# Optimization experiments

Hardware: AMD Instinct MI355X
Metric: run time of the kernel (lower is better)

Reference implementation:

```python
import jax, jax.numpy as jnp
import numpy as np

EMB = 300
NUM_LAYERS = 5
NUM_GRAPHS = 1024
NUM_JUNCTIONS = 8192
TEMP = 0.04
EPS = 1e-5
SELF_LOOP_BOND_TYPE = 4


def gcn_conv(x, edge_index, edge_attr, W, b, ee1, ee2):
    # pretrain-gnns GCNConv: add self-loops (bond type 4, direction 0),
    # degree-normalized add aggregation of (x_src + edge_emb).
    N = x.shape[0]
    loop = jnp.arange(N, dtype=edge_index.dtype)
    src = jnp.concatenate([edge_index[0], loop])
    dst = jnp.concatenate([edge_index[1], loop])
    bt = jnp.concatenate([edge_attr[:, 0], jnp.full((N,), SELF_LOOP_BOND_TYPE, edge_attr.dtype)])
    bd = jnp.concatenate([edge_attr[:, 1], jnp.zeros((N,), edge_attr.dtype)])
    eemb = ee1[bt] + ee2[bd]                                   # [E+N, D]
    deg = jax.ops.segment_sum(jnp.ones(src.shape, x.dtype), src, num_segments=N)
    dinv = jnp.where(deg > 0, 1.0 / jnp.sqrt(jnp.maximum(deg, 1e-12)), 0.0)
    norm = dinv[src] * dinv[dst]                               # [E+N]
    h = x @ W.T + b                                            # [N, D]
    msg = norm[:, None] * (h[src] + eemb)                      # gather + fuse
    return jax.ops.segment_sum(msg, dst, num_segments=N)      # scatter-add


def batchnorm(h, gamma, beta):
    mu = h.mean(0)
    var = h.var(0)
    return gamma * (h - mu) / jnp.sqrt(var + EPS) + beta


def gnn_encoder(x, edge_index, edge_attr, ae1, ae2, W, b, ee1, ee2, gamma, beta):
    h = ae1[x[:, 0]] + ae2[x[:, 1]]
    for l in range(NUM_LAYERS):
        h = gcn_conv(h, edge_index, edge_attr, W[l], b[l], ee1[l], ee2[l])
        h = batchnorm(h, gamma[l], beta[l])
        if l < NUM_LAYERS - 1:
            h = jax.nn.relu(h)
    return h


def junction_encoder(h, jW, jb, jee1, jee2):
    # SuperEncoder is called with empty edge_index -> only self-loops.
    empty_ei = jnp.zeros((2, 0), jnp.int32)
    empty_ea = jnp.zeros((0, 2), jnp.int32)
    h = jax.nn.relu(gcn_conv(h, empty_ei, empty_ea, jW[0], jb[0], jee1[0], jee2[0]))
    return gcn_conv(h, empty_ei, empty_ea, jW[1], jb[1], jee1[1], jee2[1])


def mean_pool(h, ids, num):
    s = jax.ops.segment_sum(h, ids, num_segments=num)
    c = jax.ops.segment_sum(jnp.ones((h.shape[0],), h.dtype), ids, num_segments=num)
    return s / jnp.maximum(c, 1.0)[:, None]


def l2norm(h):
    return h / jnp.maximum(jnp.linalg.norm(h, axis=1, keepdims=True), 1e-12)


def setup_inputs() -> dict:
    key = jax.random.key(0)
    ks = jax.random.split(key, 32)
    N, E = 200000, 400000
    inp = {
        'batch_x': jax.random.randint(ks[0], (N, 2), 0, 3, jnp.int32),
        'batch_edge_index': jax.random.randint(ks[1], (2, E), 0, N, jnp.int32),
        'batch_edge_attr': jax.random.randint(ks[2], (E, 2), 0, 3, jnp.int32),
        'batch_graph_ids': jax.random.randint(ks[3], (N,), 0, NUM_GRAPHS, jnp.int32),
        'frag_x': jax.random.randint(ks[4], (N, 2), 0, 3, jnp.int32),
        'frag_edge_index': jax.random.randint(ks[5], (2, E), 0, N, jnp.int32),
        'frag_edge_attr': jax.random.randint(ks[6], (E, 2), 0, 3, jnp.int32),
        'frag_junction_ids': jax.random.randint(ks[7], (N,), 0, NUM_JUNCTIONS, jnp.int32),
        'junction_graph_ids': jax.random.randint(ks[8], (NUM_JUNCTIONS,), 0, NUM_GRAPHS, jnp.int32),
        'junction_mask': jax.random.uniform(ks[9], (NUM_JUNCTIONS,), jnp.float32),
    }
    s = 0.05
    inp.update({
        'atom_emb1': jax.random.normal(ks[10], (120, EMB), jnp.float32) * s,
        'atom_emb2': jax.random.normal(ks[11], (3, EMB), jnp.float32) * s,
        'gnn_W': jax.random.normal(ks[12], (NUM_LAYERS, EMB, EMB), jnp.float32) * s,
        'gnn_b': jnp.zeros((NUM_LAYERS, EMB), jnp.float32),
        'gnn_ee1': jax.random.normal(ks[13], (NUM_LAYERS, 6, EMB), jnp.float32) * s,
        'gnn_ee2': jax.random.normal(ks[14], (NUM_LAYERS, 3, EMB), jnp.float32) * s,
        'bn_gamma': jnp.ones((NUM_LAYERS, EMB), jnp.float32),
        'bn_beta': jnp.zeros((NUM_LAYERS, EMB), jnp.float32),
        'jct_W': jax.random.normal(ks[15], (2, EMB, EMB), jnp.float32) * s,
        'jct_b': jnp.zeros((2, EMB), jnp.float32),
        'jct_ee1': jax.random.normal(ks[16], (2, 6, EMB), jnp.float32) * s,
        'jct_ee2': jax.random.normal(ks[17], (2, 3, EMB), jnp.float32) * s,
        'mask_embedding': jax.random.normal(ks[18], (EMB,), jnp.float32),
    })
    return inp


def reference(batch_x, batch_edge_index, batch_edge_attr, batch_graph_ids,
              frag_x, frag_edge_index, frag_edge_attr, frag_junction_ids,
              junction_graph_ids, junction_mask,
              atom_emb1, atom_emb2, gnn_W, gnn_b, gnn_ee1, gnn_ee2,
              bn_gamma, bn_beta, jct_W, jct_b, jct_ee1, jct_ee2, mask_embedding):
    # branch 0: whole molecules
    h = gnn_encoder(batch_x, batch_edge_index, batch_edge_attr,
                    atom_emb1, atom_emb2, gnn_W, gnn_b, gnn_ee1, gnn_ee2, bn_gamma, bn_beta)
    g = mean_pool(h, batch_graph_ids, NUM_GRAPHS)
    f0 = l2norm(junction_encoder(g, jct_W, jct_b, jct_ee1, jct_ee2))
    # branch 1: fragments -> junction nodes, masked overwrite, pooled per graph
    h = gnn_encoder(frag_x, frag_edge_index, frag_edge_attr,
                    atom_emb1, atom_emb2, gnn_W, gnn_b, gnn_ee1, gnn_ee2, bn_gamma, bn_beta)
    j = mean_pool(h, frag_junction_ids, NUM_JUNCTIONS)
    j = jnp.where(junction_mask[:, None] > 0.5, mask_embedding[None, :], j)
    j = junction_encoder(j, jct_W, jct_b, jct_ee1, jct_ee2)
    f1 = l2norm(mean_pool(j, junction_graph_ids, NUM_GRAPHS))
    logits = (f0 @ f1.T) / TEMP
    return logits
```

## Files before the change

kernel.cpp:

```cpp
#include <hip/hip_runtime.h>
#include <math.h>

#define EMBD 300
#define HROW 304
#define LDF  304
#define KEXT 320
#define BCH  80
#define BSTR 40
#define TS2  312
#define CE(a,b) (((a)+(b)-1)/(b))

typedef _Float16 h16;
typedef __attribute__((ext_vector_type(8))) _Float16 half8;
typedef __attribute__((ext_vector_type(4))) float f32x4;

__global__ void k_diag(float* out, int n, float v){
  int i = blockIdx.x*256 + threadIdx.x;
  if (i < n) out[i] = v;
}
__global__ void k_set_val(int* p, int n, int v){
  int i = blockIdx.x*256 + threadIdx.x;
  if (i < n) p[i] = v;
}
__global__ void k_count_src(const int* __restrict__ ei, int E, int* __restrict__ deg){
  int e = blockIdx.x*256 + threadIdx.x;
  if (e < E) atomicAdd(&deg[ei[e]], 1);
}
__global__ void k_dinv(const int* __restrict__ deg, float* __restrict__ dinv, int N){
  int i = blockIdx.x*256 + threadIdx.x;
  if (i < N) dinv[i] = 1.0f / sqrtf((float)(deg[i] + 1));
}
__global__ void k_count_dst(const int* __restrict__ ei, int E, int* __restrict__ counts){
  int e = blockIdx.x*256 + threadIdx.x;
  if (e < E) atomicAdd(&counts[ei[E + e]], 1);
}
__global__ void k_count_ids(const int* __restrict__ ids, int n, int* __restrict__ counts){
  int i = blockIdx.x*256 + threadIdx.x;
  if (i < n) atomicAdd(&counts[ids[i]], 1);
}
__global__ void k_scan_block(const int* __restrict__ in, int M, int* __restrict__ out, int* __restrict__ bsum){
  __shared__ int s[256];
  int t = threadIdx.x, i = blockIdx.x*256 + t;
  int v = (i < M) ? in[i] : 0;
  s[t] = v; __syncthreads();
  for (int off = 1; off < 256; off <<= 1){
    int x = (t >= off) ? s[t-off] : 0;
    __syncthreads();
    s[t] += x;
    __syncthreads();
  }
  if (i < M) out[i] = s[t] - v;
  if (t == 255) bsum[blockIdx.x] = s[255];
}
__global__ void k_scan_sums(int* __restrict__ bsum, int B){
  __shared__ int s[1024];
  int t = threadIdx.x;
  int v = (t < B) ? bsum[t] : 0;
  s[t] = v; __syncthreads();
  for (int off = 1; off < 1024; off <<= 1){
    int x = (t >= off) ? s[t-off] : 0;
    __syncthreads();
    s[t] += x;
    __syncthreads();
  }
  if (t < B) bsum[t] = s[t] - v;
}
__global__ void k_scan_add(int* __restrict__ out, const int* __restrict__ bsum, int M){
  int i = blockIdx.x*256 + threadIdx.x;
  if (i < M) out[i] += bsum[blockIdx.x];
}
__global__ void k_fill_edges(const int* __restrict__ ei, const int* __restrict__ ea, int E, int N,
                             const int* __restrict__ offs, int* __restrict__ cur, int* __restrict__ entries){
  int e = blockIdx.x*256 + threadIdx.x;
  if (e < E){
    int s  = ei[e];
    int d  = ei[E + e];
    int bt = ea[2*e], bd = ea[2*e + 1];
    int pos = offs[d] + atomicAdd(&cur[d], 1);
    entries[pos] = s | (bt << 20) | (bd << 23);
  } else if (e < E + N){
    int i = e - E;
    int pos = offs[i] + atomicAdd(&cur[i], 1);
    entries[pos] = i | (4 << 20);
  }
}
__global__ void k_fill_rows(const int* __restrict__ ids, int n, const int* __restrict__ offs,
                            int* __restrict__ cur, int* __restrict__ entries){
  int i = blockIdx.x*256 + threadIdx.x;
  if (i < n){
    int g = ids[i];
    int pos = offs[g] + atomicAdd(&cur[g], 1);
    entries[pos] = i;
  }
}

__global__ void k_init_h0(const int* __restrict__ x, const float* __restrict__ ae1,
                          const float* __restrict__ ae2, h16* __restrict__ h, int N){
  int i = blockIdx.x, t = threadIdx.x;
  int a = x[2*i], b = x[2*i + 1];
  const float* e1 = ae1 + (size_t)a*EMBD;
  const float* e2 = ae2 + (size_t)b*EMBD;
  h16* hr = h + (size_t)i*HROW;
  hr[t] = (h16)(e1[t] + e2[t]);
  int c = t + 256;
  if (c < HROW) hr[c] = (c < EMBD) ? (h16)(e1[c] + e2[c]) : (h16)0.f;
}

__global__ void k_wext(const float* __restrict__ W, const float* __restrict__ b,
                       const float* __restrict__ ee1, const float* __restrict__ ee2,
                       h16* __restrict__ out){
  int l = blockIdx.y, o = blockIdx.x, t = threadIdx.x;
  h16* d = out + ((size_t)l*KEXT + o)*KEXT;
  for (int k = t; k < KEXT; k += 256){
    float v = 0.f;
    if (o < EMBD){
      if      (k < EMBD)            v = W[(size_t)l*EMBD*EMBD + (size_t)o*EMBD + k];
      else if (k == 304)            v = b[l*EMBD + o];
      else if (k >= 305 && k < 311) v = ee1[((size_t)l*6 + (k-305))*EMBD + o];
      else if (k >= 311 && k < 314) v = ee2[((size_t)l*3 + (k-311))*EMBD + o];
    }
    d[k] = (h16)v;
  }
}

__global__ void k_id_coef(float* coef, h16* coefh){
  int c = blockIdx.x*256 + threadIdx.x;
  if (c < HROW){
    coef[c] = (c < EMBD) ? 1.f : 0.f;
    coef[HROW + c] = 0.f;
  }
  if (c < KEXT){
    coefh[c] = (c < EMBD) ? (h16)1.f : (h16)0.f;
    coefh[KEXT + c] = (h16)0.f;
  }
}
__global__ void k_bn_coef(const float* __restrict__ stats, const float* __restrict__ gamma,
                          const float* __restrict__ beta, float* __restrict__ coef,
                          h16* __restrict__ coefh, float invN){
  int c = blockIdx.x*256 + threadIdx.x;
  if (c >= KEXT) return;
  float sc = 0.f, sh = 0.f;
  if (c < EMBD){
    float mu  = stats[c]*invN;
    float var = stats[EMBD + c]*invN - mu*mu;
    sc = gamma[c]*rsqrtf(var + 1e-5f);
    sh = beta[c] - mu*sc;
  }
  if (c < HROW){ coef[c] = sc; coef[HROW + c] = sh; }
  coefh[c] = (h16)sc; coefh[KEXT + c] = (h16)sh;
}

template<int RELU>
__global__ void __launch_bounds__(256)
k_layer(const h16* __restrict__ hRaw, const h16* __restrict__ coefh,
        const float* __restrict__ dinv,
        const int* __restrict__ offs, const int* __restrict__ counts,
        const int* __restrict__ entries, const h16* __restrict__ Wx,
        h16* __restrict__ hOut, int N, float* __restrict__ stats)
{
  __shared__ h16  tile[64][TS2];
  __shared__ h16  Bs[BCH][BSTR];
  __shared__ float sred[2*HROW];
  __shared__ int   rstart[64];
  __shared__ int   rcnt[64];
  __shared__ float dvv[64];

  int tid = threadIdx.x;
  int wid = tid >> 6, lane = tid & 63;
  int m16 = lane & 15, ko = lane >> 4;
  long row0 = (long)blockIdx.x * 64;

  if (tid < 64){
    long g = row0 + tid;
    int o = 0, c = 0; float d = 0.f;
    if (g < N){ o = offs[g]; c = counts[g]; d = dinv[g]; }
    rstart[tid] = o; rcnt[tid] = c; dvv[tid] = d;
  }
  for (int i = tid; i < 2*HROW; i += 256) sred[i] = 0.f;
  __syncthreads();

  int lr = wid*16 + m16;
  int myStart = rstart[lr], myCnt = rcnt[lr];
  float di = dvv[lr];

  int srcA[8]; float wvA[8]; int eA[8];
  #pragma unroll
  for (int j = 0; j < 8; j++){
    int e = entries[myStart + j];
    bool act = j < myCnt;
    int s = act ? (e & 0xFFFFF) : N;
    float wv = dinv[act ? s : 0];
    wvA[j] = act ? wv : 0.f;
    srcA[j] = s; eA[j] = e;
  }
  float ext[8] = {0,0,0,0,0,0,0,0};
  if (ko >= 2){
    int extbase = (ko - 2)*8;
    #pragma unroll
    for (int j = 0; j < 8; j++){
      unsigned msk = 1u | (1u << (1 + ((eA[j] >> 20) & 7))) | (1u << (7 + ((eA[j] >> 23) & 3)));
      #pragma unroll
      for (int c = 0; c < 8; c++)
        ext[c] += ((msk >> (extbase + c)) & 1u) ? wvA[j] : 0.f;
    }
  }
  half8 wvh[8];
  #pragma unroll
  for (int j = 0; j < 8; j++){
    _Float16 w = (_Float16)wvA[j];
    #pragma unroll
    for (int c = 0; c < 8; c++) wvh[j][c] = w;
  }

  half8 acc[10];
  #pragma unroll
  for (int k = 0; k < 10; k++) acc[k] = (half8)(_Float16)0;

  if (__any(myCnt > 8)){
    for (int j = 8; j < myCnt; j++){
      int e = entries[myStart + j];
      int s = e & 0xFFFFF;
      float wv = dinv[s];
      if (ko >= 2){
        int extbase = (ko - 2)*8;
        unsigned msk = 1u | (1u << (1 + ((e >> 20) & 7))) | (1u << (7 + ((e >> 23) & 3)));
        #pragma unroll
        for (int c = 0; c < 8; c++)
          ext[c] += ((msk >> (extbase + c)) & 1u) ? wv : 0.f;
      }
      _Float16 wh = (_Float16)wv;
      half8 w8;
      #pragma unroll
      for (int c = 0; c < 8; c++) w8[c] = wh;
      #pragma unroll
      for (int k = 0; k < 10; k++){
        if (k == 9 && ko >= 2) break;
        half8 sck = *(const half8*)&coefh[k*32 + ko*8];
        half8 shk = *(const half8*)&coefh[KEXT + k*32 + ko*8];
        half8 x = *(const half8*)(hRaw + (size_t)s*HROW + k*32 + ko*8);
        half8 y = sck*x + shk;
        if (RELU){
          #pragma unroll
          for (int c = 0; c < 8; c++) y[c] = y[c] > (_Float16)0 ? y[c] : (_Float16)0;
        }
        acc[k] += w8*y;
      }
    }
  }

  #pragma unroll
  for (int k = 0; k < 9; k++){
    half8 sck = *(const half8*)&coefh[k*32 + ko*8];
    half8 shk = *(const half8*)&coefh[KEXT + k*32 + ko*8];
    half8 a = acc[k];
    #pragma unroll
    for (int j = 0; j < 8; j++){
      half8 x = *(const half8*)(hRaw + (size_t)srcA[j]*HROW + k*32 + ko*8);
      half8 y = sck*x + shk;
      if (RELU){
        #pragma unroll
        for (int c = 0; c < 8; c++) y[c] = y[c] > (_Float16)0 ? y[c] : (_Float16)0;
      }
      a += wvh[j]*y;
    }
    acc[k] = a;
  }
  {
    half8 a = acc[9];
    if (ko < 2){
      half8 sck = *(const half8*)&coefh[288 + ko*8];
      half8 shk = *(const half8*)&coefh[KEXT + 288 + ko*8];
      #pragma unroll
      for (int j = 0; j < 8; j++){
        half8 x = *(const half8*)(hRaw + (size_t)srcA[j]*HROW + 288 + ko*8);
        half8 y = sck*x + shk;
        if (RELU){
          #pragma unroll
          for (int c = 0; c < 8; c++) y[c] = y[c] > (_Float16)0 ? y[c] : (_Float16)0;
        }
        a += wvh[j]*y;
      }
    } else {
      #pragma unroll
      for (int c = 0; c < 8; c++) a[c] += (_Float16)ext[c];
    }
    acc[9] = a;
  }

  half8 afr[10];
  {
    _Float16 dh = (_Float16)di;
    half8 d8;
    #pragma unroll
    for (int c = 0; c < 8; c++) d8[c] = dh;
    #pragma unroll
    for (int k = 0; k < 10; k++) afr[k] = acc[k] * d8;
  }

  int cr = ko * 4;
  #pragma unroll
  for (int jt = 0; jt < 4; jt++){
    f32x4 a2[5];
    #pragma unroll
    for (int j = 0; j < 5; j++) a2[j] = (f32x4){0.f,0.f,0.f,0.f};
    for (int k0 = 0; k0 < 10; k0++){
      __syncthreads();
      for (int idx = tid; idx < 320; idx += 256){
        int o = idx >> 2, qd = (idx & 3) * 8;
        *(half8*)&Bs[o][qd] = *(const half8*)(Wx + (size_t)(jt*BCH + o)*KEXT + k0*32 + qd);
      }
      __syncthreads();
      #pragma unroll
      for (int j = 0; j < 5; j++){
        half8 bfr = *(const half8*)&Bs[j*16 + m16][ko*8];
        a2[j] = __builtin_amdgcn_mfma_f32_16x16x32_f16(afr[k0], bfr, a2[j], 0, 0, 0);
      }
    }
    #pragma unroll
    for (int j = 0; j < 5; j++){
      int col = jt*BCH + j*16 + m16;
      float s = 0.f, q = 0.f;
      #pragma unroll
      for (int r = 0; r < 4; r++){
        float v = a2[j][r];
        s += v; q += v*v;
      }
      s += __shfl_xor(s, 16, 64); s += __shfl_xor(s, 32, 64);
      q += __shfl_xor(q, 16, 64); q += __shfl_xor(q, 32, 64);
      if (ko == 0 && col < EMBD){
        atomicAdd(&sred[col], s);
        atomicAdd(&sred[HROW + col], q);
      }
    }
    #pragma unroll
    for (int j = 0; j < 5; j++){
      int col = jt*BCH + j*16 + m16;
      if (col < HROW){
        #pragma unroll
        for (int r = 0; r < 4; r++)
          tile[wid*16 + cr + r][col] = (h16)a2[j][r];
      }
    }
  }
  __syncthreads();
  for (int idx = tid; idx < 64*38; idx += 256){
    int row = idx / 38, c = idx - row*38;
    long grow = row0 + row;
    if (grow < N)
      *(uint4*)(hOut + grow*HROW + c*8) = *(const uint4*)&tile[row][c*8];
  }
  __syncthreads();
  for (int c = tid; c < EMBD; c += 256){
    atomicAdd(&stats[c], sred[c]);
    atomicAdd(&stats[EMBD + c], sred[HROW + c]);
  }
}

__global__ void k_pool_h(const h16* __restrict__ h, const int* __restrict__ offs,
                         const int* __restrict__ counts, const int* __restrict__ entries,
                         float* __restrict__ out, int M){
  int g = blockIdx.x, t = threadIdx.x, c1 = t + 256;
  int off = offs[g], cnt = counts[g];
  float a0 = 0.f, a1 = 0.f;
  for (int j = 0; j < cnt; j++){
    int r = entries[off + j];
    const h16* hr = h + (size_t)r*HROW;
    a0 += (float)hr[t];
    if (c1 < EMBD) a1 += (float)hr[c1];
  }
  float inv = 1.0f / fmaxf((float)cnt, 1.0f);
  float* o = out + (size_t)g*LDF;
  o[t] = a0*inv;
  if (c1 < EMBD) o[c1] = a1*inv;
}
__global__ void k_pool_f32(const float* __restrict__ h, const int* __restrict__ offs,
                           const int* __restrict__ counts, const int* __restrict__ entries,
                           float* __restrict__ out, int M){
  int g = blockIdx.x, t = threadIdx.x, c1 = t + 256;
  int off = offs[g], cnt = counts[g];
  float a0 = 0.f, a1 = 0.f;
  for (int j = 0; j < cnt; j++){
    int r = entries[off + j];
    const float* hr = h + (size_t)r*LDF;
    a0 += hr[t];
    if (c1 < EMBD) a1 += hr[c1];
  }
  float inv = 1.0f / fmaxf((float)cnt, 1.0f);
  float* o = out + (size_t)g*LDF;
  o[t] = a0*inv;
  if (c1 < EMBD) o[c1] = a1*inv;
}

__global__ void k_affine_rows(float* __restrict__ rows, const float* __restrict__ coef, int M){
  int g = blockIdx.x, t = threadIdx.x, c1 = t + 256;
  float* r = rows + (size_t)g*LDF;
  r[t] = coef[t]*r[t] + coef[HROW + t];
  if (c1 < EMBD) r[c1] = coef[c1]*r[c1] + coef[HROW + c1];
}

__global__ void k_mask(float* __restrict__ j, const float* __restrict__ mask,
                       const float* __restrict__ memb, int M){
  int i = blockIdx.x;
  if (mask[i] <= 0.5f) return;
  int t = threadIdx.x, c1 = t + 256;
  float* jr = j + (size_t)i*LDF;
  jr[t] = memb[t];
  if (c1 < EMBD) jr[c1] = memb[c1];
}

__global__ void k_l2norm(float* __restrict__ f, int M){
  int g = blockIdx.x, t = threadIdx.x, c1 = t + 256;
  float* fr = f + (size_t)g*LDF;
  float v0 = fr[t];
  float v1 = (c1 < EMBD) ? fr[c1] : 0.f;
  float ss = v0*v0 + v1*v1;
  #pragma unroll
  for (int o = 32; o > 0; o >>= 1) ss += __shfl_down(ss, o, 64);
  __shared__ float red[4];
  int wid = t >> 6, lane = t & 63;
  if (lane == 0) red[wid] = ss;
  __syncthreads();
  if (t == 0) red[0] = 1.0f / fmaxf(sqrtf(red[0]+red[1]+red[2]+red[3]), 1e-12f);
  __syncthreads();
  float inv = red[0];
  fr[t] = v0*inv;
  if (c1 < EMBD) fr[c1] = v1*inv;
}

__global__ void __launch_bounds__(256)
k_gemm(const float* __restrict__ A, int lda, const float* __restrict__ W, int ldw,
       const float* __restrict__ bias, const float* __restrict__ e1, const float* __restrict__ e2,
       float* __restrict__ C, int ldc, int M, int Ncols, int K, int relu, float scale){
  __shared__ float As[16][68];
  __shared__ float Ws[16][68];
  int row0 = blockIdx.y * 64, col0 = blockIdx.x * 64;
  int tid = threadIdx.x;
  int tx = tid & 15, ty = tid >> 4;
  float acc[4][4] = {};
  for (int k0 = 0; k0 < K; k0 += 16){
    int r  = tid >> 2;
    int kk = (tid & 3) * 4;
    int gk = k0 + kk;
    float v[4] = {0.f,0.f,0.f,0.f};
    int gr = row0 + r;
    if (gr < M){
      if (gk + 3 < K){ float4 f = *(const float4*)(A + (size_t)gr*lda + gk); v[0]=f.x;v[1]=f.y;v[2]=f.z;v[3]=f.w; }
      else for (int j = 0; j < 4; j++) if (gk + j < K) v[j] = A[(size_t)gr*lda + gk + j];
    }
    As[kk+0][r]=v[0]; As[kk+1][r]=v[1]; As[kk+2][r]=v[2]; As[kk+3][r]=v[3];
    float w[4] = {0.f,0.f,0.f,0.f};
    int o = col0 + r;
    if (o < Ncols){
      if (gk + 3 < K){ float4 f = *(const float4*)(W + (size_t)o*ldw + gk); w[0]=f.x;w[1]=f.y;w[2]=f.z;w[3]=f.w; }
      else for (int j = 0; j < 4; j++) if (gk + j < K) w[j] = W[(size_t)o*ldw + gk + j];
    }
    Ws[kk+0][r]=w[0]; Ws[kk+1][r]=w[1]; Ws[kk+2][r]=w[2]; Ws[kk+3][r]=w[3];
    __syncthreads();
    #pragma unroll
    for (int k = 0; k < 16; k++){
      float4 a4 = *(const float4*)&As[k][ty*4];
      float4 b4 = *(const float4*)&Ws[k][tx*4];
      float a[4] = {a4.x,a4.y,a4.z,a4.w};
      float b[4] = {b4.x,b4.y,b4.z,b4.w};
      #pragma unroll
      for (int i = 0; i < 4; i++)
        #pragma unroll
        for (int j = 0; j < 4; j++) acc[i][j] += a[i]*b[j];
    }
    __syncthreads();
  }
  #pragma unroll
  for (int i = 0; i < 4; i++){
    int rr = row0 + ty*4 + i;
    if (rr >= M) continue;
    #pragma unroll
    for (int j = 0; j < 4; j++){
      int cc = col0 + tx*4 + j;
      if (cc >= Ncols) continue;
      float v = acc[i][j];
      if (bias) v += bias[cc];
      if (e1)   v += e1[cc];
      if (e2)   v += e2[cc];
      v *= scale;
      if (relu) v = fmaxf(v, 0.f);
      C[(size_t)rr*ldc + cc] = v;
    }
  }
}

static inline void scan_excl(const int* counts, int M, int* offs, int* bsum, hipStream_t s){
  int B = CE(M, 256);
  k_scan_block<<<B,256,0,s>>>(counts, M, offs, bsum);
  k_scan_sums<<<1,1024,0,s>>>(bsum, B);
  k_scan_add<<<B,256,0,s>>>(offs, bsum, M);
}
static inline void gemm_f32(const float* A,int lda,const float* W,int ldw,
                            const float* bias,const float* e1,const float* e2,
                            float* C,int ldc,int M,int Ncols,int K,
                            int relu,float scale,hipStream_t s){
  dim3 grid(CE(Ncols,64), CE(M,64));
  k_gemm<<<grid,256,0,s>>>(A,lda,W,ldw,bias,e1,e2,C,ldc,M,Ncols,K,relu,scale);
}

extern "C" void kernel_launch(void* const* d_in, const int* in_sizes, int n_in,
                              void* d_out, int out_size, void* d_ws, size_t ws_size,
                              hipStream_t stream) {
  const int*   batch_x   = (const int*)d_in[0];
  const int*   batch_ei  = (const int*)d_in[1];
  const int*   batch_ea  = (const int*)d_in[2];
  const int*   batch_gid = (const int*)d_in[3];
  const int*   frag_x    = (const int*)d_in[4];
  const int*   frag_ei   = (const int*)d_in[5];
  const int*   frag_ea   = (const int*)d_in[6];
  const int*   frag_jid  = (const int*)d_in[7];
  const int*   jct_gid   = (const int*)d_in[8];
  const float* jct_mask  = (const float*)d_in[9];
  const float* ae1       = (const float*)d_in[10];
  const float* ae2       = (const float*)d_in[11];
  const float* gnn_W     = (const float*)d_in[12];
  const float* gnn_b     = (const float*)d_in[13];
  const float* gnn_ee1   = (const float*)d_in[14];
  const float* gnn_ee2   = (const float*)d_in[15];
  const float* bn_gamma  = (const float*)d_in[16];
  const float* bn_beta   = (const float*)d_in[17];
  const float* jct_W     = (const float*)d_in[18];
  const float* jct_b     = (const float*)d_in[19];
  const float* jct_ee1   = (const float*)d_in[20];
  const float* jct_ee2   = (const float*)d_in[21];
  const float* mask_emb  = (const float*)d_in[22];

  const int N = in_sizes[0] / 2;
  const int E = in_sizes[1] / 2;
  const int NG = 1024, NJ = 8192;

  size_t off = 0;
  char* base = (char*)d_ws;
  auto carve = [&](size_t bytes) -> void* {
    void* p = base + off;
    off += (bytes + 255) & ~(size_t)255;
    return p;
  };
  h16*  hA      = (h16*) carve((size_t)(N+1) * HROW * 2);
  h16*  hB      = (h16*) carve((size_t)(N+1) * HROW * 2);
  float* dinv    = (float*)carve((size_t)N * 4);
  int*   degcnt  = (int*)  carve((size_t)N * 4);
  int*   cursor  = degcnt;
  int*   counts  = (int*)  carve((size_t)N * 4);
  int*   offs    = (int*)  carve((size_t)(N + 1) * 4);
  int*   entries = (int*)  carve((size_t)(E + N) * 4);
  int*   bsum    = (int*)  carve(1024 * 4);
  float* stats   = (float*)carve(2 * EMBD * 4);
  float* coef    = (float*)carve(2 * HROW * 4);
  float* idcoef  = (float*)carve(2 * HROW * 4);
  h16*  coefh   = (h16*) carve(2 * KEXT * 2);
  h16*  idcoefh = (h16*) carve(2 * KEXT * 2);
  h16*  wext    = (h16*) carve((size_t)5 * KEXT * KEXT * 2);
  float* f0      = (float*)carve((size_t)NG * LDF * 4);
  float* f1      = (float*)carve((size_t)NG * LDF * 4);
  size_t required = off;
  float* g0      = (float*)hA;
  float* t1      = (float*)((char*)hA + ((size_t)16 << 20));
  float* t2      = (float*)((char*)hA + ((size_t)32 << 20));
  (void)n_in;

  if (ws_size < required || d_ws == nullptr){
    float v = 1.0e6f + (float)(ws_size >> 20) * 1000.0f;
    k_diag<<<CE(out_size,256),256,0,stream>>>((float*)d_out, out_size, v);
    return;
  }

  { dim3 g(KEXT, 5); k_wext<<<g,256,0,stream>>>(gnn_W, gnn_b, gnn_ee1, gnn_ee2, wext); }
  k_id_coef<<<CE(KEXT,256),256,0,stream>>>(idcoef, idcoefh);
  hipMemsetAsync(hA + (size_t)N*HROW, 0, HROW*2, stream);
  hipMemsetAsync(hB + (size_t)N*HROW, 0, HROW*2, stream);

  const int LBLK = CE(N, 64);

  for (int br = 0; br < 2; br++){
    const int* x  = br ? frag_x  : batch_x;
    const int* ei = br ? frag_ei : batch_ei;
    const int* ea = br ? frag_ea : batch_ea;

    hipMemsetAsync(degcnt, 0, (size_t)N*4, stream);
    k_count_src<<<CE(E,256),256,0,stream>>>(ei, E, degcnt);
    k_dinv<<<CE(N,256),256,0,stream>>>(degcnt, dinv, N);

    k_set_val<<<CE(N,256),256,0,stream>>>(counts, N, 1);
    k_count_dst<<<CE(E,256),256,0,stream>>>(ei, E, counts);
    scan_excl(counts, N, offs, bsum, stream);
    hipMemsetAsync(cursor, 0, (size_t)N*4, stream);
    k_fill_edges<<<CE(E+N,256),256,0,stream>>>(ei, ea, E, N, offs, cursor, entries);

    k_init_h0<<<N,256,0,stream>>>(x, ae1, ae2, hA, N);

    for (int l = 0; l < 5; l++){
      const h16* src = (l & 1) ? hB : hA;
      h16*       dst = (l & 1) ? hA : hB;
      const h16* ch  = (l == 0) ? idcoefh : coefh;
      hipMemsetAsync(stats, 0, 2*EMBD*4, stream);
      if (l == 0)
        k_layer<0><<<LBLK,256,0,stream>>>(src, ch, dinv, offs, counts, entries,
                                          wext + (size_t)l*KEXT*KEXT, dst, N, stats);
      else
        k_layer<1><<<LBLK,256,0,stream>>>(src, ch, dinv, offs, counts, entries,
                                          wext + (size_t)l*KEXT*KEXT, dst, N, stats);
      k_bn_coef<<<CE(KEXT,256),256,0,stream>>>(stats, bn_gamma + l*EMBD, bn_beta + l*EMBD,
                                               coef, coefh, 1.0f/(float)N);
    }

    if (br == 0){
      hipMemsetAsync(counts, 0, (size_t)NG*4, stream);
      k_count_ids<<<CE(N,256),256,0,stream>>>(batch_gid, N, counts);
      scan_excl(counts, NG, offs, bsum, stream);
      hipMemsetAsync(cursor, 0, (size_t)NG*4, stream);
      k_fill_rows<<<CE(N,256),256,0,stream>>>(batch_gid, N, offs, cursor, entries);
      k_pool_h<<<NG,256,0,stream>>>(hB, offs, counts, entries, g0, NG);
      k_affine_rows<<<NG,256,0,stream>>>(g0, coef, NG);
      gemm_f32(g0, LDF, jct_W, EMBD, jct_b,
               jct_ee1 + 4*EMBD, jct_ee2,
               t1, LDF, NG, EMBD, EMBD, 1, 1.0f, stream);
      gemm_f32(t1, LDF, jct_W + EMBD*EMBD, EMBD, jct_b + EMBD,
               jct_ee1 + 6*EMBD + 4*EMBD, jct_ee2 + 3*EMBD,
               f0, LDF, NG, EMBD, EMBD, 0, 1.0f, stream);
      k_l2norm<<<NG,256,0,stream>>>(f0, NG);
    } else {
      hipMemsetAsync(counts, 0, (size_t)NJ*4, stream);
      k_count_ids<<<CE(N,256),256,0,stream>>>(frag_jid, N, counts);
      scan_excl(counts, NJ, offs, bsum, stream);
      hipMemsetAsync(cursor, 0, (size_t)NJ*4, stream);
      k_fill_rows<<<CE(N,256),256,0,stream>>>(frag_jid, N, offs, cursor, entries);
      k_pool_h<<<NJ,256,0,stream>>>(hB, offs, counts, entries, t1, NJ);
      k_affine_rows<<<NJ,256,0,stream>>>(t1, coef, NJ);
      k_mask<<<NJ,256,0,stream>>>(t1, jct_mask, mask_emb, NJ);
      gemm_f32(t1, LDF, jct_W, EMBD, jct_b,
               jct_ee1 + 4*EMBD, jct_ee2,
               t2, LDF, NJ, EMBD, EMBD, 1, 1.0f, stream);
      gemm_f32(t2, LDF, jct_W + EMBD*EMBD, EMBD, jct_b + EMBD,
               jct_ee1 + 6*EMBD + 4*EMBD, jct_ee2 + 3*EMBD,
               t1, LDF, NJ, EMBD, EMBD, 0, 1.0f, stream);
      hipMemsetAsync(counts, 0, (size_t)NG*4, stream);
      k_count_ids<<<CE(NJ,256),256,0,stream>>>(jct_gid, NJ, counts);
      scan_excl(counts, NG, offs, bsum, stream);
      hipMemsetAsync(cursor, 0, (size_t)NG*4, stream);
      k_fill_rows<<<CE(NJ,256),256,0,stream>>>(jct_gid, NJ, offs, cursor, entries);
      k_pool_f32<<<NG,256,0,stream>>>(t1, offs, counts, entries, f1, NG);
      k_l2norm<<<NG,256,0,stream>>>(f1, NG);
    }
  }

  gemm_f32(f0, LDF, f1, LDF, nullptr, nullptr, nullptr,
           (float*)d_out, 1024, NG, NG, EMBD, 0, 25.0f, stream);
}
```

Baseline: 4.075 ms.

## Read GEMM weight fragments directly from global memory and shrink LDS tile

The layer kernel no longer stages weight chunks through shared memory with two barriers per k-step. Each lane now loads its B fragment straight from global memory, relying on cache reuse across waves. The output tile is packed to 300 columns, writes use 8-byte stores with zero padding, and the per-row metadata is read directly rather than staged. Less LDS should allow higher occupancy and fewer barriers, at the cost of more global and L2 traffic, uncoalesced weight loads and possible LDS bank conflicts from the 300 stride.

```diff
diff --git a/kernel.cpp b/kernel.cpp
--- a/kernel.cpp
+++ b/kernel.cpp
@@ -6,8 +6,6 @@
 #define LDF  304
 #define KEXT 320
 #define BCH  80
-#define BSTR 40
-#define TS2  312
 #define CE(a,b) (((a)+(b)-1)/(b))
 
 typedef _Float16 h16;
@@ -158,30 +156,21 @@
         const int* __restrict__ entries, const h16* __restrict__ Wx,
         h16* __restrict__ hOut, int N, float* __restrict__ stats)
 {
-  __shared__ h16  tile[64][TS2];
-  __shared__ h16  Bs[BCH][BSTR];
-  __shared__ float sred[2*HROW];
-  __shared__ int   rstart[64];
-  __shared__ int   rcnt[64];
-  __shared__ float dvv[64];
+  __shared__ h16  tile[64*300];
+  __shared__ float sred[600];
 
   int tid = threadIdx.x;
   int wid = tid >> 6, lane = tid & 63;
   int m16 = lane & 15, ko = lane >> 4;
   long row0 = (long)blockIdx.x * 64;
 
-  if (tid < 64){
-    long g = row0 + tid;
-    int o = 0, c = 0; float d = 0.f;
-    if (g < N){ o = offs[g]; c = counts[g]; d = dinv[g]; }
-    rstart[tid] = o; rcnt[tid] = c; dvv[tid] = d;
-  }
-  for (int i = tid; i < 2*HROW; i += 256) sred[i] = 0.f;
+  for (int i = tid; i < 600; i += 256) sred[i] = 0.f;
   __syncthreads();
 
   int lr = wid*16 + m16;
-  int myStart = rstart[lr], myCnt = rcnt[lr];
-  float di = dvv[lr];
+  long g = row0 + lr;
+  int myStart = 0, myCnt = 0; float di = 0.f;
+  if (g < N){ myStart = offs[g]; myCnt = counts[g]; di = dinv[g]; }
 
   int srcA[8]; float wvA[8]; int eA[8];
   #pragma unroll
@@ -298,21 +287,14 @@
   }
 
   int cr = ko * 4;
-  #pragma unroll
   for (int jt = 0; jt < 4; jt++){
     f32x4 a2[5];
     #pragma unroll
     for (int j = 0; j < 5; j++) a2[j] = (f32x4){0.f,0.f,0.f,0.f};
     for (int k0 = 0; k0 < 10; k0++){
-      __syncthreads();
-      for (int idx = tid; idx < 320; idx += 256){
-        int o = idx >> 2, qd = (idx & 3) * 8;
-        *(half8*)&Bs[o][qd] = *(const half8*)(Wx + (size_t)(jt*BCH + o)*KEXT + k0*32 + qd);
-      }
-      __syncthreads();
       #pragma unroll
       for (int j = 0; j < 5; j++){
-        half8 bfr = *(const half8*)&Bs[j*16 + m16][ko*8];
+        half8 bfr = *(const half8*)(Wx + (size_t)(jt*BCH + j*16 + m16)*KEXT + k0*32 + ko*8);
         a2[j] = __builtin_amdgcn_mfma_f32_16x16x32_f16(afr[k0], bfr, a2[j], 0, 0, 0);
       }
     }
@@ -329,30 +311,28 @@
       q += __shfl_xor(q, 16, 64); q += __shfl_xor(q, 32, 64);
       if (ko == 0 && col < EMBD){
         atomicAdd(&sred[col], s);
-        atomicAdd(&sred[HROW + col], q);
-      }
-    }
-    #pragma unroll
-    for (int j = 0; j < 5; j++){
-      int col = jt*BCH + j*16 + m16;
-      if (col < HROW){
+        atomicAdd(&sred[300 + col], q);
+      }
+      if (col < EMBD){
         #pragma unroll
         for (int r = 0; r < 4; r++)
-          tile[wid*16 + cr + r][col] = (h16)a2[j][r];
+          tile[(wid*16 + cr + r)*300 + col] = (h16)a2[j][r];
       }
     }
   }
   __syncthreads();
-  for (int idx = tid; idx < 64*38; idx += 256){
-    int row = idx / 38, c = idx - row*38;
+  for (int idx = tid; idx < 64*76; idx += 256){
+    int row = idx / 76, c = idx - row*76;
     long grow = row0 + row;
-    if (grow < N)
-      *(uint4*)(hOut + grow*HROW + c*8) = *(const uint4*)&tile[row][c*8];
-  }
-  __syncthreads();
+    if (grow < N){
+      uint2 v = make_uint2(0u, 0u);
+      if (c < 75) v = *(const uint2*)&tile[row*300 + c*4];
+      *(uint2*)(hOut + grow*HROW + c*4) = v;
+    }
+  }
   for (int c = tid; c < EMBD; c += 256){
     atomicAdd(&stats[c], sred[c]);
-    atomicAdd(&stats[EMBD + c], sred[HROW + c]);
+    atomicAdd(&stats[EMBD + c], sred[300 + c]);
   }
 }
 
```

Result: slower. 5.513 ms (+35.3%).
